# Performance work log

Measured on AMD Instinct MI355X. Metric: run time of the kernel, lower is better.

The kernel has to match this reference:

```python
import jax, jax.numpy as jnp
import numpy as np

EPS = 1e-5
K = 16
DILATION = 1

def _bn(x, g, b, axes):
    # BatchNorm in training mode: batch statistics over all axes except channel (last)
    m = jnp.mean(x, axis=axes, keepdims=True)
    v = jnp.var(x, axis=axes, keepdims=True)
    return (x - m) * jax.lax.rsqrt(v + EPS) * g + b

def _knn_idx(p, q, k):
    # p: [B,N,3], q: [B,M,3] -> indices [B,M,k] of nearest points in p for each q
    d = (jnp.sum(q * q, -1)[:, :, None]
         - 2.0 * jnp.einsum('bmc,bnc->bmn', q, p)
         + jnp.sum(p * p, -1)[:, None, :])  # [B,M,N]
    _, idx = jax.lax.top_k(-d, k)
    return jax.lax.stop_gradient(idx)

def setup_inputs() -> dict:
    key = jax.random.key(0)
    ks = jax.random.split(key, 16)
    B, N, M, Cin, Cout = 8, 8192, 2048, 64, 128
    mid, K2 = Cout // 4, K * K
    s = 0.02
    d = {
        'p': jax.random.normal(ks[0], (B, N, 3), jnp.float32),
        'q': jax.random.normal(ks[1], (B, M, 3), jnp.float32),
        'x': jax.random.normal(ks[2], (B, Cin, N), jnp.float32),
        # mlp: two 1x1 convs (3->mid->mid) each with BN
        'W1': jax.random.normal(ks[3], (mid, 3), jnp.float32) * s,
        'b1': jnp.zeros((mid,), jnp.float32),
        'g1': jnp.ones((mid,), jnp.float32), 'be1': jnp.zeros((mid,), jnp.float32),
        'W2': jax.random.normal(ks[4], (mid, mid), jnp.float32) * s,
        'b2': jnp.zeros((mid,), jnp.float32),
        'g2': jnp.ones((mid,), jnp.float32), 'be2': jnp.zeros((mid,), jnp.float32),
        # stn: conv [1,K] (3->K^2), then two 1x1 convs (K^2->K^2)
        'Ws1': jax.random.normal(ks[5], (K2, 3, K), jnp.float32) * s,
        'bs1': jnp.zeros((K2,), jnp.float32),
        'gs1': jnp.ones((K2,), jnp.float32), 'bes1': jnp.zeros((K2,), jnp.float32),
        'Ws2': jax.random.normal(ks[6], (K2, K2), jnp.float32) * s,
        'bs2': jnp.zeros((K2,), jnp.float32),
        'gs2': jnp.ones((K2,), jnp.float32), 'bes2': jnp.zeros((K2,), jnp.float32),
        'Ws3': jax.random.normal(ks[7], (K2, K2), jnp.float32) * s,
        'bs3': jnp.zeros((K2,), jnp.float32),
        # final conv [1,K]: (Cin+mid -> Cout) with BN
        'Wc': jax.random.normal(ks[8], (Cout, Cin + mid, K), jnp.float32) * s,
        'bc': jnp.zeros((Cout,), jnp.float32),
        'gc': jnp.ones((Cout,), jnp.float32), 'bec': jnp.zeros((Cout,), jnp.float32),
    }
    return d

def reference(p, q, x, W1, b1, g1, be1, W2, b2, g2, be2,
              Ws1, bs1, gs1, bes1, Ws2, bs2, gs2, bes2, Ws3, bs3,
              Wc, bc, gc, bec):
    B, M = q.shape[0], q.shape[1]
    idx = _knn_idx(p, q, K * DILATION)[..., ::DILATION]  # [B,M,K]
    # gather neighbor coords and center: p_hat [B,M,K,3]
    p_n = jax.vmap(lambda a, i: a[i])(p, idx)
    p_hat = p_n - q[:, :, None, :]
    # mlp (pointwise convs, channel-last)
    h = jax.nn.relu(_bn(jnp.einsum('bmkc,oc->bmko', p_hat, W1) + b1, g1, be1, (0, 1, 2)))
    h = jax.nn.relu(_bn(jnp.einsum('bmkc,oc->bmko', h, W2) + b2, g2, be2, (0, 1, 2)))
    # gather features: x [B,Cin,N] -> [B,M,K,Cin]
    xt = jnp.transpose(x, (0, 2, 1))
    x_n = jax.vmap(lambda a, i: a[i])(xt, idx)
    x_hat = jnp.concatenate([h, x_n], axis=-1)  # [B,M,K,mid+Cin]
    # stn -> transform T [B,M,K,K]
    t = jax.nn.relu(_bn(jnp.einsum('bmkc,ock->bmo', p_hat, Ws1) + bs1, gs1, bes1, (0, 1)))
    t = jax.nn.relu(_bn(jnp.einsum('bmi,oi->bmo', t, Ws2) + bs2, gs2, bes2, (0, 1)))
    t = jnp.einsum('bmi,oi->bmo', t, Ws3) + bs3  # [B,M,K*K]
    T = t.reshape(B, M, K, K)
    x2 = jnp.einsum('bmij,bmjc->bmic', T, x_hat)  # [B,M,K,mid+Cin]
    out = jax.nn.relu(_bn(jnp.einsum('bmkc,ock->bmo', x2, Wc) + bc, gc, bec, (0, 1)))  # [B,M,Cout]
    return (q, jnp.transpose(out, (0, 2, 1)))  # q, x:[B,Cout,M]
```

## Files before the change

kernel.cpp:

```cpp
#include <hip/hip_runtime.h>
#include <hip/hip_bf16.h>


#define EPS 1e-5f

constexpr int Bb   = 8;
constexpr int Np   = 8192;
constexpr int Mq   = 2048;
constexpr int COUT = 128;
constexpr int BM   = Bb * Mq;
constexpr int BMK  = BM * 16;
constexpr int GC   = 16;
constexpr int NC   = GC * GC * GC;
constexpr int CAP  = 320;
constexpr int TS   = 20;

typedef __attribute__((ext_vector_type(8))) short short8;
typedef __attribute__((ext_vector_type(4))) float f32x4;

__device__ __forceinline__ unsigned short f2bf(float x) {
  unsigned u = __float_as_uint(x);
  u += 0x7fffu + ((u >> 16) & 1u);
  return (unsigned short)(u >> 16);
}
__device__ __forceinline__ float bf2f_lo(unsigned v) { return __uint_as_float(v << 16); }
__device__ __forceinline__ float bf2f_hi(unsigned v) { return __uint_as_float(v & 0xffff0000u); }
__device__ __forceinline__ float bfround(float x) {
  return __uint_as_float(((unsigned)f2bf(x)) << 16);
}

__device__ __forceinline__ int cell_of(float c) {
  int v = (int)floorf(c * 2.0f + 8.0f);
  return v < 0 ? 0 : (v > 15 ? 15 : v);
}

__device__ __forceinline__ unsigned enc_dist(float d) {
  unsigned uu = __float_as_uint(d);
  return uu ^ (((unsigned)(((int)uu) >> 31)) | 0x80000000u);
}

__device__ __forceinline__ void bsort64(unsigned long long& v, int lane) {
#pragma unroll
  for (int k = 2; k <= 64; k <<= 1) {
#pragma unroll
    for (int jj = k >> 1; jj > 0; jj >>= 1) {
      unsigned long long o = __shfl_xor(v, jj);
      bool keepMin = (((lane & k) == 0) == ((lane & jj) == 0));
      unsigned long long mn = v < o ? v : o;
      unsigned long long mx = v < o ? o : v;
      v = keepMin ? mn : mx;
    }
  }
}
__device__ __forceinline__ void bmerge64(unsigned long long& v, int lane) {
#pragma unroll
  for (int jj = 32; jj > 0; jj >>= 1) {
    unsigned long long o = __shfl_xor(v, jj);
    bool keepMin = ((lane & jj) == 0);
    unsigned long long mn = v < o ? v : o;
    unsigned long long mx = v < o ? o : v;
    v = keepMin ? mn : mx;
  }
}
__device__ __forceinline__ unsigned long long sort_smallest64(const unsigned long long* buf,
                                                              int C, int lane) {
  unsigned long long run = (lane < C) ? buf[lane] : ~0ULL;
  bsort64(run, lane);
  for (int b2 = 64; b2 < C; b2 += 64) {
    unsigned long long v = (b2 + lane < C) ? buf[b2 + lane] : ~0ULL;
    bsort64(v, lane);
    unsigned long long vr = __shfl_xor(v, 63);
    unsigned long long m = run < vr ? run : vr;
    bmerge64(m, lane);
    run = m;
  }
  return run;
}


__device__ __forceinline__ void bn1_compute(int o, const float* __restrict__ st,
                                            const float* __restrict__ W1,
                                            const float* __restrict__ b1,
                                            const float* __restrict__ g1,
                                            const float* __restrict__ be1,
                                            float* sc_out, float* shf_out) {
  float n = (float)BMK;
  float w0 = W1[3 * o], w1 = W1[3 * o + 1], w2 = W1[3 * o + 2], b = b1[o];
  float s0 = st[0], s1 = st[1], s2 = st[2];
  float m00 = st[3], m11 = st[4], m22 = st[5], m01 = st[6], m02 = st[7], m12 = st[8];
  float ws = (w0 * s0 + w1 * s1 + w2 * s2) / n;
  float mean = b + ws;
  float quad = w0 * w0 * m00 + w1 * w1 * m11 + w2 * w2 * m22 +
               2.f * (w0 * w1 * m01 + w0 * w2 * m02 + w1 * w2 * m12);
  float ex2 = quad / n + 2.f * b * ws + b * b;
  float var = ex2 - mean * mean;
  float sc = g1[o] * rsqrtf(var + EPS);
  *sc_out = sc;
  *shf_out = be1[o] - mean * sc + b * sc;
}

__global__ __launch_bounds__(256) void prep_kernel(const float* __restrict__ p,
                                                   const float* __restrict__ x,
                                                   const float* __restrict__ Wc,
                                                   const float* __restrict__ Ws1,
                                                   float4* __restrict__ pp4,
                                                   float* __restrict__ xt,
                                                   unsigned short* __restrict__ wcrp,
                                                   unsigned short* __restrict__ ws1r,
                                                   int* __restrict__ hist) {
  __shared__ float tile[64][65];
  int blk = blockIdx.x;
  int tid = threadIdx.x;
  if (blk < 256) {
    int i = blk * 256 + tid;
    float px = p[3 * i], py = p[3 * i + 1], pz = p[3 * i + 2];
    float pp = __fadd_rn(__fadd_rn(__fmul_rn(px, px), __fmul_rn(py, py)), __fmul_rn(pz, pz));
    pp4[i] = make_float4(px, py, pz, pp);
    int b = i >> 13;
    int cid = (cell_of(px) << 8) | (cell_of(py) << 4) | cell_of(pz);
    atomicAdd(&hist[b * NC + cid], 1);
  } else if (blk < 1280) {
    int bx = blk - 256;
    int b = bx >> 7;
    int n0 = (bx & 127) << 6;
    int nl = tid & 63;
    int r0 = tid >> 6;
    const float* xb = x + (size_t)b * 64 * Np;
    for (int c = r0; c < 64; c += 4) tile[c][nl] = xb[(size_t)c * Np + n0 + nl];
    __syncthreads();
    float* xtb = xt + (size_t)b * Np * 64;
    for (int n = r0; n < 64; n += 4) xtb[(size_t)(n0 + n) * 64 + nl] = tile[nl][n];
  } else if (blk < 2048) {
    int g = (blk - 1280) * 256 + tid;
    if (g < 128 * 1536) {
      int o = g / 1536, r = g % 1536;
      int c = r % 96, j = r / 96;
      wcrp[g] = f2bf(Wc[(size_t)o * 1536 + c * 16 + j]);
    }
  } else {
    int g = (blk - 2048) * 256 + tid;
    int o = g >> 6, i = g & 63;
    float val = 0.f;
    if (i < 48) {
      int k = i / 3, c = i - 3 * k;
      val = Ws1[(size_t)o * 48 + c * 16 + k];
    }
    unsigned short h = f2bf(val);
    float hf = __uint_as_float(((unsigned)h) << 16);
    unsigned short l = f2bf(val - hf);
    ws1r[g] = h;
    ws1r[16384 + g] = l;
  }
}

__global__ __launch_bounds__(256) void prefix_kernel(const int* __restrict__ hist,
                                                     int* __restrict__ cellstart,
                                                     int* __restrict__ cursor) {
  __shared__ int ls[256];
  int b = blockIdx.x, t = threadIdx.x;
  const int* h = hist + b * NC;
  int loc[16], s = 0;
#pragma unroll
  for (int k = 0; k < 16; ++k) { loc[k] = h[t * 16 + k]; s += loc[k]; }
  ls[t] = s;
  __syncthreads();
  for (int off = 1; off < 256; off <<= 1) {
    int v = (t >= off) ? ls[t - off] : 0;
    __syncthreads();
    ls[t] += v;
    __syncthreads();
  }
  int run = ls[t] - s;
  int* cs = cellstart + b * (NC + 1);
  int* cu = cursor + b * NC;
#pragma unroll
  for (int k = 0; k < 16; ++k) {
    cs[t * 16 + k] = run;
    cu[t * 16 + k] = run;
    run += loc[k];
  }
  if (t == 255) cs[NC] = run;
}

__global__ __launch_bounds__(256) void scatter_kernel(const float4* __restrict__ pp4,
                                                      int* __restrict__ cursor,
                                                      float4* __restrict__ sp4,
                                                      int* __restrict__ sidx) {
  int i = blockIdx.x * 256 + threadIdx.x;
  int b = i >> 13;
  float4 pv = pp4[i];
  int cid = (cell_of(pv.x) << 8) | (cell_of(pv.y) << 4) | cell_of(pv.z);
  int pos = atomicAdd(&cursor[b * NC + cid], 1);
  sp4[(size_t)b * Np + pos] = pv;
  sidx[(size_t)b * Np + pos] = i & 8191;
}

__global__ __launch_bounds__(256) void knn_kernel(const float4* __restrict__ pp4,
                                                  const float4* __restrict__ sp4,
                                                  const int* __restrict__ sidx,
                                                  const int* __restrict__ cellstart,
                                                  const float* __restrict__ q,
                                                  int* __restrict__ idx_out) {
  __shared__ unsigned long long cand[4][CAP];
  int tid = threadIdx.x;
  int wslot = tid >> 6;
  int qi = blockIdx.x * 4 + wslot;
  int lane = tid & 63;
  int b = qi >> 11;
  const float4* pb = pp4 + (size_t)b * Np;
  const float4* sp = sp4 + (size_t)b * Np;
  const int* sx = sidx + (size_t)b * Np;
  const int* cs = cellstart + b * (NC + 1);
  const float* qp = q + (size_t)qi * 3;
  float qx = qp[0], qy = qp[1], qz = qp[2];
  float qqv = __fadd_rn(__fadd_rn(__fmul_rn(qx, qx), __fmul_rn(qy, qy)), __fmul_rn(qz, qz));
  float tau_f = INFINITY;

  {
    int cx = cell_of(qx), cy = cell_of(qy), cz = cell_of(qz);
    int alo = 0, blo = 0, nbw = 1, ncols = 1, zlo = 0, zhi = 0;
    int myS = 0, myE = 0;
    for (int r = 0;; ++r) {
      alo = cx - r; if (alo < 0) alo = 0;
      int ahi = cx + r; if (ahi > 15) ahi = 15;
      blo = cy - r; if (blo < 0) blo = 0;
      int bhi = cy + r; if (bhi > 15) bhi = 15;
      zlo = cz - r; if (zlo < 0) zlo = 0;
      zhi = cz + r; if (zhi > 15) zhi = 15;
      nbw = bhi - blo + 1;
      ncols = (ahi - alo + 1) * nbw;
      int total = 0;
      for (int l0 = 0; l0 < ncols; l0 += 64) {
        int l = l0 + lane;
        int sL = 0, eL = 0;
        if (l < ncols) {
          int da = l / nbw, db = l - da * nbw;
          int cbase = ((alo + da) << 8) | ((blo + db) << 4);
          sL = cs[cbase + zlo];
          eL = cs[cbase + zhi + 1];
        }
        if (l0 == 0) { myS = sL; myE = eL; }
        total += eL - sL;
      }
#pragma unroll
      for (int o = 32; o > 0; o >>= 1) total += __shfl_xor(total, o);
      if (total >= 16 || r >= 15) break;
    }
    unsigned u0 = 0xFFFFFFFFu, u1 = 0xFFFFFFFFu;
    int wcnt = 0;
    int ccen = (cx - alo) * nbw + (cy - blo);
    for (int c2 = 0; c2 < ncols && wcnt < 128; ++c2) {
      int cc = (c2 == 0) ? ccen : (c2 <= ccen ? c2 - 1 : c2);
      int s0, e;
      if (cc < 64) {
        s0 = __shfl(myS, cc);
        e = __shfl(myE, cc);
      } else {
        int da = cc / nbw, db = cc - da * nbw;
        int cbase = ((alo + da) << 8) | ((blo + db) << 4);
        s0 = cs[cbase + zlo];
        e = cs[cbase + zhi + 1];
      }
      for (int off = s0; off < e && wcnt < 128; off += 64) {
        int rem = e - off; if (rem > 64) rem = 64;
        int rot = wcnt & 63;
        int rel = (lane - rot) & 63;
        int g = wcnt + rel;
        if (rel < rem && g < 128) {
          float4 pv = sp[off + rel];
          float ee = __fmaf_rn(qz, pv.z, __fmaf_rn(qy, pv.y, __fmul_rn(qx, pv.x)));
          float d = __fadd_rn(__fsub_rn(qqv, __fmul_rn(2.0f, ee)), pv.w);
          unsigned uu = enc_dist(d);
          if (g < 64) u0 = uu; else u1 = uu;
        }
        wcnt += rem;
      }
    }
    unsigned lo = 0u, hi = 0xFF800000u;
    for (int it = 0; it < 20; ++it) {
      unsigned mid = lo + ((hi - lo) >> 1);
      int c = (int)__popcll(__ballot(u0 <= mid)) + (int)__popcll(__ballot(u1 <= mid));
      if (c >= 16) hi = mid; else lo = mid + 1;
    }
    tau_f = (hi >= 0x80000000u) ? __uint_as_float(hi ^ 0x80000000u)
                                : __uint_as_float(~hi);
  }

  int cnt = 0;
  unsigned long long lanebelow = (1ULL << lane) - 1ULL;
  {
    float R = sqrtf(fmaxf(tau_f, 0.f) + 3e-5f) * 1.0005f;
    int ax0 = cell_of(qx - R), ax1 = cell_of(qx + R);
    int ay0 = cell_of(qy - R), ay1 = cell_of(qy + R);
    int az0 = cell_of(qz - R), az1 = cell_of(qz + R);
    int nby = ay1 - ay0 + 1;
    int ncols = (ax1 - ax0 + 1) * nby;
    int myS = 0, myE = 0;
    if (lane < ncols) {
      int da = lane / nby, db = lane - da * nby;
      int cbase = ((ax0 + da) << 8) | ((ay0 + db) << 4);
      myS = cs[cbase + az0];
      myE = cs[cbase + az1 + 1];
    }
    for (int cc = 0; cc < ncols; ++cc) {
      int s0, e;
      if (cc < 64) {
        s0 = __shfl(myS, cc);
        e = __shfl(myE, cc);
      } else {
        int da = cc / nby, db = cc - da * nby;
        int cbase = ((ax0 + da) << 8) | ((ay0 + db) << 4);
        s0 = cs[cbase + az0];
        e = cs[cbase + az1 + 1];
      }
      for (int off = s0; off < e; off += 64) {
        int pos = off + lane;
        bool valid = pos < e;
        float4 pv = sp[valid ? pos : s0];
        float ee = __fmaf_rn(qz, pv.z, __fmaf_rn(qy, pv.y, __fmul_rn(qx, pv.x)));
        float d = __fadd_rn(__fsub_rn(qqv, __fmul_rn(2.0f, ee)), pv.w);
        if (!valid) d = __uint_as_float(0x7FC00000u);
        unsigned long long mask = __ballot(d <= tau_f);
        if (mask) {
          if (d <= tau_f) {
            int oi = sx[pos];
            unsigned uu = enc_dist(d);
            int wp = cnt + (int)__popcll(mask & lanebelow);
            if (wp < CAP)
              cand[wslot][wp] = (((unsigned long long)uu) << 32) | (unsigned)oi;
          }
          cnt += (int)__popcll(mask);
        }
      }
    }
  }
  __syncthreads();

  if (cnt <= CAP) {
    unsigned long long run = sort_smallest64(&cand[wslot][0], cnt, lane);
    if (lane < 16)
      idx_out[(size_t)qi * 16 + lane] = (int)(run & 0xffffffffULL);
  } else {
    unsigned long long kk = ~0ULL;
    float tl = tau_f;
    for (int base = 0; base < Np; base += 64) {
      float4 pv = pb[base + lane];
      float ee = __fmaf_rn(qz, pv.z, __fmaf_rn(qy, pv.y, __fmul_rn(qx, pv.x)));
      float dv = __fadd_rn(__fsub_rn(qqv, __fmul_rn(2.0f, ee)), pv.w);
      unsigned long long mask = __ballot(dv <= tl);
      if (mask) {
        unsigned uu = enc_dist(dv);
        unsigned long long cd = (((unsigned long long)uu) << 32) | (unsigned)(base + lane);
        do {
          int src = __ffsll((unsigned long long)mask) - 1;
          mask &= mask - 1;
          unsigned long long ck = __shfl(cd, src);
          unsigned long long up = __shfl_up(kk, 1);
          if (lane == 0) up = 0ULL;
          if (lane < 16 && ck < kk) kk = (up > ck) ? up : ck;
        } while (mask);
        unsigned long long tt = __shfl(kk, 15);
        unsigned tm = (unsigned)(tt >> 32);
        unsigned inv2 = tm ^ ((tm & 0x80000000u) ? 0x80000000u : 0xFFFFFFFFu);
        float tc = (tm == 0xFFFFFFFFu) ? INFINITY : __uint_as_float(inv2);
        if (tc < tl) tl = tc;
      }
    }
    if (lane < 16)
      idx_out[(size_t)qi * 16 + lane] = (int)(kk & 0xffffffffULL);
  }
}

__global__ __launch_bounds__(256) void phat_stats_kernel(const float4* __restrict__ pp4,
                                                         const float* __restrict__ q,
                                                         const int* __restrict__ idx,
                                                         float* __restrict__ phat,
                                                         float* __restrict__ stats) {
  float a[9];
#pragma unroll
  for (int k = 0; k < 9; ++k) a[k] = 0.f;
  int tid = threadIdx.x;
  for (int it = 0; it < 4; ++it) {
    int bmk = blockIdx.x * 256 + tid + it * 65536;
    int bm = bmk >> 4;
    int b = bm >> 11;
    int j = idx[bmk];
    float4 pv = pp4[(size_t)b * Np + j];
    const float* qp = q + (size_t)bm * 3;
    float h0 = pv.x - qp[0], h1 = pv.y - qp[1], h2 = pv.z - qp[2];
    phat[(size_t)bmk * 3 + 0] = h0;
    phat[(size_t)bmk * 3 + 1] = h1;
    phat[(size_t)bmk * 3 + 2] = h2;
    a[0] += h0; a[1] += h1; a[2] += h2;
    a[3] += h0 * h0; a[4] += h1 * h1; a[5] += h2 * h2;
    a[6] += h0 * h1; a[7] += h0 * h2; a[8] += h1 * h2;
  }
#pragma unroll
  for (int off = 32; off > 0; off >>= 1)
#pragma unroll
    for (int k = 0; k < 9; ++k) a[k] += __shfl_down(a[k], off);
  __shared__ float ls[9];
  if (tid < 9) ls[tid] = 0.f;
  __syncthreads();
  if ((tid & 63) == 0)
    for (int k = 0; k < 9; ++k) atomicAdd(&ls[k], a[k]);
  __syncthreads();
  if (tid < 9) atomicAdd(&stats[tid], ls[tid]);
}

__global__ __launch_bounds__(256) void stats2_kernel(const float* __restrict__ phat,
                                                     const float* __restrict__ stats,
                                                     const float* __restrict__ W1,
                                                     const float* __restrict__ b1,
                                                     const float* __restrict__ g1,
                                                     const float* __restrict__ be1,
                                                     const float* __restrict__ W2,
                                                     const float* __restrict__ b2,
                                                     float* __restrict__ stats2) {
  __shared__ float hsh[256 * 36];
  __shared__ float w2s[32 * 33];
  __shared__ float w1s[96], sc1[32], sh1[32], b2s[32], ls[64];
  int tid = threadIdx.x;
  if (tid < 32) {
    bn1_compute(tid, stats, W1, b1, g1, be1, &sc1[tid], &sh1[tid]);
    b2s[tid] = b2[tid];
  }
  if (tid < 96) w1s[tid] = W1[tid];
  if (tid < 64) ls[tid] = 0.f;
  for (int e = tid; e < 1024; e += 256) w2s[(e >> 5) * 33 + (e & 31)] = W2[e];
  __syncthreads();
  {
    int bmk = blockIdx.x * 256 + tid;
    float h0 = phat[(size_t)bmk * 3], hy = phat[(size_t)bmk * 3 + 1], hz = phat[(size_t)bmk * 3 + 2];
#pragma unroll
    for (int o4 = 0; o4 < 8; ++o4) {
      float4 r;
      float* rp = (float*)&r;
#pragma unroll
      for (int u = 0; u < 4; ++u) {
        int o = o4 * 4 + u;
        float t = w1s[3 * o] * h0 + w1s[3 * o + 1] * hy + w1s[3 * o + 2] * hz;
        rp[u] = fmaxf(0.f, t * sc1[o] + sh1[o]);
      }
      *(float4*)&hsh[tid * 36 + o4 * 4] = r;
    }
  }
  __syncthreads();
  int oc = tid & 31, grp = tid >> 5;
  float wrow[32];
#pragma unroll
  for (int c = 0; c < 32; ++c) wrow[c] = w2s[oc * 33 + c];
  float bias = b2s[oc];
  float ss = 0.f, qq = 0.f;
  for (int r = 0; r < 32; ++r) {
    int row = grp * 32 + r;
    float a = bias;
    const float4* hr = (const float4*)&hsh[row * 36];
#pragma unroll
    for (int c4 = 0; c4 < 8; ++c4) {
      float4 hv = hr[c4];
      a += hv.x * wrow[c4 * 4 + 0];
      a += hv.y * wrow[c4 * 4 + 1];
      a += hv.z * wrow[c4 * 4 + 2];
      a += hv.w * wrow[c4 * 4 + 3];
    }
    ss += a;
    qq += a * a;
  }
  atomicAdd(&ls[oc], ss);
  atomicAdd(&ls[32 + oc], qq);
  __syncthreads();
  if (tid < 64) atomicAdd(&stats2[tid], ls[tid]);
}

__global__ __launch_bounds__(256) void stn1_kernel(const float* __restrict__ phat,
                                                   const unsigned short* __restrict__ ws1r,
                                                   const float* __restrict__ bs1,
                                                   float* __restrict__ pt1,
                                                   float* __restrict__ spt1) {
  __shared__ unsigned short Ah[64 * 72], Al[64 * 72], Bh[128 * 72], Bl[128 * 72];
  __shared__ float ls[256];
  int tid = threadIdx.x;
  ls[tid] = 0.f;
  int mb = blockIdx.x >> 1, nb = blockIdx.x & 1;
  int bm0 = mb * 64, o0 = nb * 128;
  {
    int zr = tid >> 2, zc = 48 + (tid & 3) * 4;
    *(unsigned long long*)&Ah[zr * 72 + zc] = 0ULL;
    *(unsigned long long*)&Al[zr * 72 + zc] = 0ULL;
  }
  {
    int ar = tid >> 2, aseg = tid & 3;
    const float* Ap = phat + (size_t)(bm0 + ar) * 48 + aseg * 12;
    float4 v0 = *(const float4*)(Ap);
    float4 v1 = *(const float4*)(Ap + 4);
    float4 v2 = *(const float4*)(Ap + 8);
    float av[12] = {v0.x, v0.y, v0.z, v0.w, v1.x, v1.y, v1.z, v1.w, v2.x, v2.y, v2.z, v2.w};
    unsigned long long ph[3] = {0ULL, 0ULL, 0ULL}, pl[3] = {0ULL, 0ULL, 0ULL};
#pragma unroll
    for (int t = 0; t < 12; ++t) {
      unsigned short h = f2bf(av[t]);
      float hf = __uint_as_float(((unsigned)h) << 16);
      unsigned short l = f2bf(av[t] - hf);
      ph[t >> 2] |= ((unsigned long long)h) << ((t & 3) * 16);
      pl[t >> 2] |= ((unsigned long long)l) << ((t & 3) * 16);
    }
    int base = ar * 72 + aseg * 12;
#pragma unroll
    for (int t4 = 0; t4 < 3; ++t4) {
      *(unsigned long long*)&Ah[base + t4 * 4] = ph[t4];
      *(unsigned long long*)&Al[base + t4 * 4] = pl[t4];
    }
  }
#pragma unroll
  for (int pass = 0; pass < 4; ++pass) {
    int g = pass * 2048 + tid * 8;
    int br = g >> 6, i2 = g & 63;
    short8 vh = *(const short8*)&ws1r[(size_t)(o0 + br) * 64 + i2];
    short8 vl = *(const short8*)&ws1r[16384 + (size_t)(o0 + br) * 64 + i2];
    *(short8*)&Bh[br * 72 + i2] = vh;
    *(short8*)&Bl[br * 72 + i2] = vl;
  }
  __syncthreads();
  int wid = tid >> 6, lane = tid & 63;
  int wm = wid >> 1, wn = wid & 1;
  int mh = lane & 15, quad = lane >> 4;
  f32x4 acc[2][4];
#pragma unroll
  for (int a = 0; a < 2; ++a)
#pragma unroll
    for (int bq = 0; bq < 4; ++bq) acc[a][bq] = (f32x4){0.f, 0.f, 0.f, 0.f};
#pragma unroll
  for (int kc = 0; kc < 2; ++kc) {
    int ko = kc * 32 + quad * 8;
#pragma unroll
    for (int mt = 0; mt < 2; ++mt) {
      short8 ah = *(const short8*)&Ah[(wm * 32 + mt * 16 + mh) * 72 + ko];
      short8 al = *(const short8*)&Al[(wm * 32 + mt * 16 + mh) * 72 + ko];
#pragma unroll
      for (int nt = 0; nt < 4; ++nt) {
        short8 bh = *(const short8*)&Bh[(wn * 64 + nt * 16 + mh) * 72 + ko];
        short8 bl = *(const short8*)&Bl[(wn * 64 + nt * 16 + mh) * 72 + ko];
        acc[mt][nt] = __builtin_amdgcn_mfma_f32_16x16x32_bf16(ah, bh, acc[mt][nt], 0, 0, 0);
        acc[mt][nt] = __builtin_amdgcn_mfma_f32_16x16x32_bf16(ah, bl, acc[mt][nt], 0, 0, 0);
        acc[mt][nt] = __builtin_amdgcn_mfma_f32_16x16x32_bf16(al, bh, acc[mt][nt], 0, 0, 0);
      }
    }
  }
#pragma unroll
  for (int mt = 0; mt < 2; ++mt)
#pragma unroll
    for (int nt = 0; nt < 4; ++nt) {
      int colL = wn * 64 + nt * 16 + mh;
      int col = o0 + colL;
      float bvv = bs1[col];
      float ps = 0.f, pq = 0.f;
#pragma unroll
      for (int r = 0; r < 4; ++r) {
        float val = acc[mt][nt][r] + bvv;
        pt1[(size_t)(bm0 + wm * 32 + mt * 16 + quad * 4 + r) * 256 + col] = val;
        ps += val;
        pq += val * val;
      }
      atomicAdd(&ls[colL], ps);
      atomicAdd(&ls[128 + colL], pq);
    }
  __syncthreads();
  if (tid < 128) {
    atomicAdd(&spt1[o0 + tid], ls[tid]);
    atomicAdd(&spt1[256 + o0 + tid], ls[128 + tid]);
  }
}

__global__ __launch_bounds__(256) void stn_mm_kernel(const float* __restrict__ in,
                                                     const float* __restrict__ sums,
                                                     const float* __restrict__ gg,
                                                     const float* __restrict__ be,
                                                     const float* __restrict__ W,
                                                     const float* __restrict__ bias,
                                                     float* __restrict__ out,
                                                     float* __restrict__ outstats,
                                                     int do_stats) {
  __shared__ unsigned short As[64 * 40], Bs[128 * 40];
  __shared__ float scA[256], shA[256], ls[256];
  int tid = threadIdx.x;
  ls[tid] = 0.f;
  {
    float n = (float)BM;
    float mean = sums[tid] / n;
    float var = sums[256 + tid] / n - mean * mean;
    float s = gg[tid] * rsqrtf(var + EPS);
    scA[tid] = s;
    shA[tid] = be[tid] - mean * s;
  }
  int mb = blockIdx.x >> 1, nb = blockIdx.x & 1;
  int bm0 = mb * 64, o0 = nb * 128;
  int wid = tid >> 6, lane = tid & 63;
  int wm = wid >> 1, wn = wid & 1;
  int mh = lane & 15, quad = lane >> 4;
  f32x4 acc[2][4];
#pragma unroll
  for (int a = 0; a < 2; ++a)
#pragma unroll
    for (int bq = 0; bq < 4; ++bq) acc[a][bq] = (f32x4){0.f, 0.f, 0.f, 0.f};
  int ar = tid >> 2, aseg = tid & 3;
  const float* Ag = in + (size_t)(bm0 + ar) * 256 + aseg * 8;
  int aoff = ar * 40 + aseg * 8;
  int ci = aseg * 8;
  for (int i0 = 0; i0 < 256; i0 += 32) {
    __syncthreads();
    float4 v0 = *(const float4*)(Ag + i0);
    float4 v1 = *(const float4*)(Ag + i0 + 4);
    float av[8] = {v0.x, v0.y, v0.z, v0.w, v1.x, v1.y, v1.z, v1.w};
    short8 ap;
#pragma unroll
    for (int k = 0; k < 8; ++k)
      ap[k] = (short)f2bf(fmaxf(0.f, av[k] * scA[i0 + ci + k] + shA[i0 + ci + k]));
    *(short8*)&As[aoff] = ap;
#pragma unroll
    for (int jb = 0; jb < 2; ++jb) {
      int br = jb * 64 + ar;
      const float* Bg = W + (size_t)(o0 + br) * 256 + aseg * 8;
      float4 u0 = *(const float4*)(Bg + i0);
      float4 u1 = *(const float4*)(Bg + i0 + 4);
      float bv[8] = {u0.x, u0.y, u0.z, u0.w, u1.x, u1.y, u1.z, u1.w};
      short8 bp;
#pragma unroll
      for (int k = 0; k < 8; ++k) bp[k] = (short)f2bf(bv[k]);
      *(short8*)&Bs[br * 40 + aseg * 8] = bp;
    }
    __syncthreads();
#pragma unroll
    for (int mt = 0; mt < 2; ++mt) {
      short8 af = *(const short8*)&As[(wm * 32 + mt * 16 + mh) * 40 + quad * 8];
#pragma unroll
      for (int nt = 0; nt < 4; ++nt) {
        short8 bf = *(const short8*)&Bs[(wn * 64 + nt * 16 + mh) * 40 + quad * 8];
        acc[mt][nt] = __builtin_amdgcn_mfma_f32_16x16x32_bf16(af, bf, acc[mt][nt], 0, 0, 0);
      }
    }
  }
#pragma unroll
  for (int mt = 0; mt < 2; ++mt)
#pragma unroll
    for (int nt = 0; nt < 4; ++nt) {
      int colL = wn * 64 + nt * 16 + mh;
      int col = o0 + colL;
      float bvv = bias[col];
      float ps = 0.f, pq = 0.f;
#pragma unroll
      for (int r = 0; r < 4; ++r) {
        float val = acc[mt][nt][r] + bvv;
        out[(size_t)(bm0 + wm * 32 + mt * 16 + quad * 4 + r) * 256 + col] = val;
        ps += val;
        pq += val * val;
      }
      if (do_stats) {
        atomicAdd(&ls[colL], ps);
        atomicAdd(&ls[128 + colL], pq);
      }
    }
  if (do_stats) {
    __syncthreads();
    if (tid < 128) {
      atomicAdd(&outstats[o0 + tid], ls[tid]);
      atomicAdd(&outstats[256 + o0 + tid], ls[128 + tid]);
    }
  }
}

__global__ __launch_bounds__(256) void xhat_x2_kernel(const float* __restrict__ phat,
                                                      const float* __restrict__ stats,
                                                      const float* __restrict__ stats2,
                                                      const float* __restrict__ W1,
                                                      const float* __restrict__ b1,
                                                      const float* __restrict__ g1,
                                                      const float* __restrict__ be1,
                                                      const float* __restrict__ W2,
                                                      const float* __restrict__ b2,
                                                      const float* __restrict__ g2,
                                                      const float* __restrict__ be2,
                                                      const float* __restrict__ xt,
                                                      const int* __restrict__ idx,
                                                      const float* __restrict__ Tbuf,
                                                      unsigned short* __restrict__ x2) {
  __shared__ unsigned xh[256 * 17];
  __shared__ float Tst[256 * TS];
  __shared__ float sc1[32], sh1[32], sc2[32], sh2[32];
  int tid = threadIdx.x;
  if (tid < 32) {
    bn1_compute(tid, stats, W1, b1, g1, be1, &sc1[tid], &sh1[tid]);
    float n = (float)BMK;
    float mean = stats2[tid] / n;
    float var = stats2[32 + tid] / n - mean * mean;
    float s = g2[tid] * rsqrtf(var + EPS);
    sc2[tid] = s;
    sh2[tid] = be2[tid] - mean * s + b2[tid] * s;
  }
  __syncthreads();
  int bm0 = blockIdx.x * 16;
  int b = bm0 >> 11;
  int bml = tid >> 4, j = tid & 15;
  int bmk = (bm0 + bml) * 16 + j;
  int jxr[16];
  {
    const int* idxrow = idx + (size_t)(bm0 + bml) * 16;
#pragma unroll
    for (int jj = 0; jj < 16; ++jj) jxr[jj] = idxrow[jj];
  }
  {
    float h0 = phat[(size_t)bmk * 3], hy = phat[(size_t)bmk * 3 + 1], hz = phat[(size_t)bmk * 3 + 2];
    float h1v[32];
#pragma unroll
    for (int o = 0; o < 32; ++o) {
      float t = W1[3 * o] * h0 + W1[3 * o + 1] * hy + W1[3 * o + 2] * hz;
      h1v[o] = fmaxf(0.f, t * sc1[o] + sh1[o]);
    }
#pragma unroll
    for (int o4 = 0; o4 < 8; ++o4) {
      float r[4];
#pragma unroll
      for (int u = 0; u < 4; ++u) {
        int o = o4 * 4 + u;
        float a = 0.f;
#pragma unroll
        for (int c = 0; c < 32; ++c) a += h1v[c] * W2[o * 32 + c];
        r[u] = fmaxf(0.f, a * sc2[o] + sh2[o]);
      }
      xh[tid * 17 + o4 * 2] = (unsigned)f2bf(r[0]) | (((unsigned)f2bf(r[1])) << 16);
      xh[tid * 17 + o4 * 2 + 1] = (unsigned)f2bf(r[2]) | (((unsigned)f2bf(r[3])) << 16);
    }
    const float4* tg = (const float4*)(Tbuf + (size_t)(bm0 + bml) * 256 + j * 16);
    float4* td = (float4*)&Tst[tid * TS];
    td[0] = tg[0]; td[1] = tg[1]; td[2] = tg[2]; td[3] = tg[3];
  }
  __syncthreads();
  int cl = j;
  {
    float vlo[16], vhi[16];
#pragma unroll
    for (int jj = 0; jj < 16; ++jj) {
      unsigned uv = xh[(bml * 16 + jj) * 17 + cl];
      vlo[jj] = bf2f_lo(uv);
      vhi[jj] = bf2f_hi(uv);
    }
    for (int jo = 0; jo < 16; ++jo) {
      const float4* tr4 = (const float4*)&Tst[(bml * 16 + jo) * TS];
      float4 ta = tr4[0], tb = tr4[1], tc = tr4[2], tdd = tr4[3];
      float trow[16] = {ta.x, ta.y, ta.z, ta.w, tb.x, tb.y, tb.z, tb.w,
                        tc.x, tc.y, tc.z, tc.w, tdd.x, tdd.y, tdd.z, tdd.w};
      float a0 = 0.f, a1 = 0.f;
#pragma unroll
      for (int jj = 0; jj < 16; ++jj) {
        a0 += trow[jj] * vlo[jj];
        a1 += trow[jj] * vhi[jj];
      }
      unsigned* dst = (unsigned*)(x2 + (size_t)((bm0 + bml) * 16 + jo) * 96);
      dst[cl] = (unsigned)f2bf(a0) | (((unsigned)f2bf(a1)) << 16);
    }
  }
  {
    float v0[16], v1[16], v2[16], v3[16];
#pragma unroll
    for (int jj = 0; jj < 16; ++jj) {
      int jx = jxr[jj];
      float4 xv = *(const float4*)(xt + ((size_t)b * Np + jx) * 64 + cl * 4);
      v0[jj] = bfround(xv.x);
      v1[jj] = bfround(xv.y);
      v2[jj] = bfround(xv.z);
      v3[jj] = bfround(xv.w);
    }
    for (int jo = 0; jo < 16; ++jo) {
      const float4* tr4 = (const float4*)&Tst[(bml * 16 + jo) * TS];
      float4 ta = tr4[0], tb = tr4[1], tc = tr4[2], tdd = tr4[3];
      float trow[16] = {ta.x, ta.y, ta.z, ta.w, tb.x, tb.y, tb.z, tb.w,
                        tc.x, tc.y, tc.z, tc.w, tdd.x, tdd.y, tdd.z, tdd.w};
      float a0 = 0.f, a1 = 0.f, a2 = 0.f, a3 = 0.f;
#pragma unroll
      for (int jj = 0; jj < 16; ++jj) {
        float t = trow[jj];
        a0 += t * v0[jj];
        a1 += t * v1[jj];
        a2 += t * v2[jj];
        a3 += t * v3[jj];
      }
      unsigned* dst = (unsigned*)(x2 + (size_t)((bm0 + bml) * 16 + jo) * 96);
      dst[16 + cl * 2] = (unsigned)f2bf(a0) | (((unsigned)f2bf(a1)) << 16);
      dst[17 + cl * 2] = (unsigned)f2bf(a2) | (((unsigned)f2bf(a3)) << 16);
    }
  }
}

__global__ __launch_bounds__(256) void preout_kernel(const unsigned short* __restrict__ x2,
                                                     const unsigned short* __restrict__ Wcrp,
                                                     const float* __restrict__ bc,
                                                     float* __restrict__ pout,
                                                     float* __restrict__ spout) {
  __shared__ unsigned short As[64 * 40], Bs[128 * 40];
  __shared__ float ls[256];
  int tid = threadIdx.x;
  ls[tid] = 0.f;
  int bm0 = blockIdx.x * 64;
  int wid = tid >> 6, lane = tid & 63;
  int wm = wid >> 1, wn = wid & 1;
  int mh = lane & 15, quad = lane >> 4;
  f32x4 acc[2][4];
#pragma unroll
  for (int a = 0; a < 2; ++a)
#pragma unroll
    for (int bq = 0; bq < 4; ++bq) acc[a][bq] = (f32x4){0.f, 0.f, 0.f, 0.f};
  int ar = tid >> 2, aseg = tid & 3;
  const unsigned short* Ag = x2 + (size_t)(bm0 + ar) * 1536 + aseg * 8;
  const unsigned short* Bg0 = Wcrp + (size_t)ar * 1536 + aseg * 8;
  const unsigned short* Bg1 = Wcrp + (size_t)(64 + ar) * 1536 + aseg * 8;
  int aoff = ar * 40 + aseg * 8;
  short8 a_pre = *(const short8*)Ag;
  short8 b_pre0 = *(const short8*)Bg0;
  short8 b_pre1 = *(const short8*)Bg1;
  for (int i0 = 0; i0 < 1536; i0 += 32) {
    __syncthreads();
    *(short8*)&As[aoff] = a_pre;
    *(short8*)&Bs[aoff] = b_pre0;
    *(short8*)&Bs[64 * 40 + aoff] = b_pre1;
    __syncthreads();
    if (i0 + 32 < 1536) {
      a_pre = *(const short8*)(Ag + i0 + 32);
      b_pre0 = *(const short8*)(Bg0 + i0 + 32);
      b_pre1 = *(const short8*)(Bg1 + i0 + 32);
    }
#pragma unroll
    for (int mt = 0; mt < 2; ++mt) {
      short8 af = *(const short8*)&As[(wm * 32 + mt * 16 + mh) * 40 + quad * 8];
#pragma unroll
      for (int nt = 0; nt < 4; ++nt) {
        short8 bf = *(const short8*)&Bs[(wn * 64 + nt * 16 + mh) * 40 + quad * 8];
        acc[mt][nt] = __builtin_amdgcn_mfma_f32_16x16x32_bf16(af, bf, acc[mt][nt], 0, 0, 0);
      }
    }
  }
#pragma unroll
  for (int mt = 0; mt < 2; ++mt)
#pragma unroll
    for (int nt = 0; nt < 4; ++nt) {
      int col = wn * 64 + nt * 16 + mh;
      float bvv = bc[col];
      float ps = 0.f, pq = 0.f;
#pragma unroll
      for (int r = 0; r < 4; ++r) {
        float val = acc[mt][nt][r] + bvv;
        pout[(size_t)(bm0 + wm * 32 + mt * 16 + quad * 4 + r) * 128 + col] = val;
        ps += val;
        pq += val * val;
      }
      atomicAdd(&ls[col], ps);
      atomicAdd(&ls[128 + col], pq);
    }
  __syncthreads();
  atomicAdd(&spout[tid], ls[tid]);
}

__global__ __launch_bounds__(256) void final_kernel(const float* __restrict__ q,
                                                    const float* __restrict__ pout,
                                                    const float* __restrict__ scs,
                                                    const float* __restrict__ gc,
                                                    const float* __restrict__ bec,
                                                    float* __restrict__ dout) {
  __shared__ float ldsT[128 * 65];
  int blk = blockIdx.x;
  int tid = threadIdx.x;
  if (blk < 192) {
    int g = blk * 256 + tid;
    dout[g] = q[g];
    return;
  }
  int blk2 = blk - 192;
  int b = blk2 >> 5;
  int m0 = (blk2 & 31) * 64;
  int row = tid >> 2, seg = tid & 3;
  const float4* src = (const float4*)(pout + ((size_t)(b * Mq) + m0 + row) * 128 + seg * 32);
#pragma unroll
  for (int k4 = 0; k4 < 8; ++k4) {
    float4 v = src[k4];
    int o = seg * 32 + k4 * 4;
    ldsT[(o + 0) * 65 + row] = v.x;
    ldsT[(o + 1) * 65 + row] = v.y;
    ldsT[(o + 2) * 65 + row] = v.z;
    ldsT[(o + 3) * 65 + row] = v.w;
  }
  __syncthreads();
  int lane = tid & 63, wv = tid >> 6;
  float n = (float)BM;
  float* base = dout + (size_t)BM * 3 + (size_t)b * COUT * Mq + m0;
#pragma unroll
  for (int rep = 0; rep < 32; ++rep) {
    int o = wv * 32 + rep;
    float mean = scs[o] / n;
    float var = scs[128 + o] / n - mean * mean;
    float s = gc[o] * rsqrtf(var + EPS);
    float shv = bec[o] - mean * s;
    float v = ldsT[o * 65 + lane];
    base[(size_t)o * Mq + lane] = fmaxf(0.f, v * s + shv);
  }
}

extern "C" void kernel_launch(void* const* d_in, const int* in_sizes, int n_in, void* d_out,
                              int out_size, void* d_ws, size_t ws_size, hipStream_t stream) {
  const float* p = (const float*)d_in[0];
  const float* q = (const float*)d_in[1];
  const float* x = (const float*)d_in[2];
  const float* W1 = (const float*)d_in[3];
  const float* b1 = (const float*)d_in[4];
  const float* g1 = (const float*)d_in[5];
  const float* be1 = (const float*)d_in[6];
  const float* W2 = (const float*)d_in[7];
  const float* b2 = (const float*)d_in[8];
  const float* g2 = (const float*)d_in[9];
  const float* be2 = (const float*)d_in[10];
  const float* Ws1 = (const float*)d_in[11];
  const float* bs1 = (const float*)d_in[12];
  const float* gs1 = (const float*)d_in[13];
  const float* bes1 = (const float*)d_in[14];
  const float* Ws2 = (const float*)d_in[15];
  const float* bs2 = (const float*)d_in[16];
  const float* gs2 = (const float*)d_in[17];
  const float* bes2 = (const float*)d_in[18];
  const float* Ws3 = (const float*)d_in[19];
  const float* bs3 = (const float*)d_in[20];
  const float* Wc = (const float*)d_in[21];
  const float* bc = (const float*)d_in[22];
  const float* gc = (const float*)d_in[23];
  const float* bec = (const float*)d_in[24];
  float* dout = (float*)d_out;

  char* ws = (char*)d_ws;
  float* stats = (float*)ws;
  size_t off = 8192;
  float4* pp4 = (float4*)(ws + off);  off += (size_t)Bb * Np * 16;
  int* idxb = (int*)(ws + off);       off += (size_t)BMK * 4;
  float* xt = (float*)(ws + off);     off += (size_t)Bb * Np * 64 * 4;
  float* phat = (float*)(ws + off);   off += (size_t)BMK * 3 * 4;
  float* pt1 = (float*)(ws + off);    off += (size_t)BM * 256 * 4;
  float* pt2 = (float*)(ws + off);    off += (size_t)BM * 256 * 4;
  float* Tb = (float*)(ws + off);     off += (size_t)BM * 256 * 4;
  float* pout = (float*)(ws + off);   off += (size_t)BM * 128 * 4;
  unsigned short* wcrp = (unsigned short*)(ws + off); off += (size_t)1536 * 128 * 2;
  unsigned short* x2 = (unsigned short*)(ws + off);   off += (size_t)BM * 1536 * 2;
  int* hist = (int*)(ws + off);       off += (size_t)Bb * NC * 4;
  int* cursor = (int*)(ws + off);     off += (size_t)Bb * NC * 4;
  int* cellstart = (int*)(ws + off);  off += (size_t)Bb * (NC + 1) * 4;
  float4* sp4 = (float4*)(ws + off);  off += (size_t)Bb * Np * 16;
  int* sidx = (int*)(ws + off);       off += (size_t)Bb * Np * 4;
  unsigned short* ws1r = (unsigned short*)(ws + off); off += (size_t)2 * 256 * 64 * 2;

  hipMemsetAsync(stats, 0, 8192, stream);
  hipMemsetAsync(hist, 0, (size_t)Bb * NC * 4, stream);
  hipLaunchKernelGGL(prep_kernel, dim3(2112), dim3(256), 0, stream, p, x, Wc, Ws1, pp4, xt, wcrp, ws1r, hist);
  hipLaunchKernelGGL(prefix_kernel, dim3(8), dim3(256), 0, stream, hist, cellstart, cursor);
  hipLaunchKernelGGL(scatter_kernel, dim3(256), dim3(256), 0, stream, pp4, cursor, sp4, sidx);
  hipLaunchKernelGGL(knn_kernel, dim3(4096), dim3(256), 0, stream, pp4, sp4, sidx, cellstart, q, idxb);
  hipLaunchKernelGGL(phat_stats_kernel, dim3(256), dim3(256), 0, stream, pp4, q, idxb, phat, stats);
  hipLaunchKernelGGL(stn1_kernel, dim3(512), dim3(256), 0, stream, phat, ws1r, bs1, pt1, stats + 128);
  hipLaunchKernelGGL(stats2_kernel, dim3(1024), dim3(256), 0, stream, phat, stats, W1, b1, g1, be1, W2, b2, stats + 16);
  hipLaunchKernelGGL(stn_mm_kernel, dim3(512), dim3(256), 0, stream, pt1, stats + 128, gs1, bes1, Ws2, bs2, pt2, stats + 640, 1);
  hipLaunchKernelGGL(stn_mm_kernel, dim3(512), dim3(256), 0, stream, pt2, stats + 640, gs2, bes2, Ws3, bs3, Tb, (float*)nullptr, 0);
  hipLaunchKernelGGL(xhat_x2_kernel, dim3(1024), dim3(256), 0, stream, phat, stats, stats + 16,
                     W1, b1, g1, be1, W2, b2, g2, be2, xt, idxb, Tb, x2);
  hipLaunchKernelGGL(preout_kernel, dim3(256), dim3(256), 0, stream, x2, wcrp, bc, pout, stats + 1152);
  hipLaunchKernelGGL(final_kernel, dim3(448), dim3(256), 0, stream, q, pout, stats + 1152, gc, bec, dout);
}
```

Before: 355.7 us.

## Fuse phat computation into kNN, one query per block, move q copy to prep

The kNN kernel now runs one wave per block (64 threads, 16384 blocks) and computes the centred neighbour coordinates (phat) for its 16 results right away. This drops the separate gather pass in phat_stats_kernel, which now only reads phat to accumulate statistics. The copy of q into the output moves from final_kernel into extra prep_kernel blocks. Single-wave blocks remove the block-wide sync and let waves with slow queries retire independently, at the cost of more block launches and some redundant work per block.

```diff
diff --git a/kernel.cpp b/kernel.cpp
--- a/kernel.cpp
+++ b/kernel.cpp
@@ -103,11 +103,13 @@
                                                    const float* __restrict__ x,
                                                    const float* __restrict__ Wc,
                                                    const float* __restrict__ Ws1,
+                                                   const float* __restrict__ q,
                                                    float4* __restrict__ pp4,
                                                    float* __restrict__ xt,
                                                    unsigned short* __restrict__ wcrp,
                                                    unsigned short* __restrict__ ws1r,
-                                                   int* __restrict__ hist) {
+                                                   int* __restrict__ hist,
+                                                   float* __restrict__ dout) {
   __shared__ float tile[64][65];
   int blk = blockIdx.x;
   int tid = threadIdx.x;
@@ -137,7 +139,7 @@
       int c = r % 96, j = r / 96;
       wcrp[g] = f2bf(Wc[(size_t)o * 1536 + c * 16 + j]);
     }
-  } else {
+  } else if (blk < 2112) {
     int g = (blk - 2048) * 256 + tid;
     int o = g >> 6, i = g & 63;
     float val = 0.f;
@@ -150,6 +152,9 @@
     unsigned short l = f2bf(val - hf);
     ws1r[g] = h;
     ws1r[16384 + g] = l;
+  } else {
+    int g = (blk - 2112) * 256 + tid;
+    dout[g] = q[g];
   }
 }
 
@@ -195,17 +200,16 @@
   sidx[(size_t)b * Np + pos] = i & 8191;
 }
 
-__global__ __launch_bounds__(256) void knn_kernel(const float4* __restrict__ pp4,
-                                                  const float4* __restrict__ sp4,
-                                                  const int* __restrict__ sidx,
-                                                  const int* __restrict__ cellstart,
-                                                  const float* __restrict__ q,
-                                                  int* __restrict__ idx_out) {
-  __shared__ unsigned long long cand[4][CAP];
-  int tid = threadIdx.x;
-  int wslot = tid >> 6;
-  int qi = blockIdx.x * 4 + wslot;
-  int lane = tid & 63;
+__global__ __launch_bounds__(64) void knn_kernel(const float4* __restrict__ pp4,
+                                                 const float4* __restrict__ sp4,
+                                                 const int* __restrict__ sidx,
+                                                 const int* __restrict__ cellstart,
+                                                 const float* __restrict__ q,
+                                                 int* __restrict__ idx_out,
+                                                 float* __restrict__ phat) {
+  __shared__ unsigned long long cand[CAP];
+  int lane = threadIdx.x;
+  int qi = blockIdx.x;
   int b = qi >> 11;
   const float4* pb = pp4 + (size_t)b * Np;
   const float4* sp = sp4 + (size_t)b * Np;
@@ -327,19 +331,17 @@
             unsigned uu = enc_dist(d);
             int wp = cnt + (int)__popcll(mask & lanebelow);
             if (wp < CAP)
-              cand[wslot][wp] = (((unsigned long long)uu) << 32) | (unsigned)oi;
+              cand[wp] = (((unsigned long long)uu) << 32) | (unsigned)oi;
           }
           cnt += (int)__popcll(mask);
         }
       }
     }
   }
-  __syncthreads();
-
+
+  unsigned long long key16 = ~0ULL;
   if (cnt <= CAP) {
-    unsigned long long run = sort_smallest64(&cand[wslot][0], cnt, lane);
-    if (lane < 16)
-      idx_out[(size_t)qi * 16 + lane] = (int)(run & 0xffffffffULL);
+    key16 = sort_smallest64(&cand[0], cnt, lane);
   } else {
     unsigned long long kk = ~0ULL;
     float tl = tau_f;
@@ -366,15 +368,21 @@
         if (tc < tl) tl = tc;
       }
     }
-    if (lane < 16)
-      idx_out[(size_t)qi * 16 + lane] = (int)(kk & 0xffffffffULL);
-  }
-}
-
-__global__ __launch_bounds__(256) void phat_stats_kernel(const float4* __restrict__ pp4,
-                                                         const float* __restrict__ q,
-                                                         const int* __restrict__ idx,
-                                                         float* __restrict__ phat,
+    key16 = kk;
+  }
+  if (lane < 16) {
+    int oi = (int)(key16 & 0xffffffffULL);
+    idx_out[(size_t)qi * 16 + lane] = oi;
+    float4 pv = pb[oi];
+    float h0 = pv.x - qx, h1 = pv.y - qy, h2 = pv.z - qz;
+    size_t base3 = ((size_t)qi * 16 + lane) * 3;
+    phat[base3 + 0] = h0;
+    phat[base3 + 1] = h1;
+    phat[base3 + 2] = h2;
+  }
+}
+
+__global__ __launch_bounds__(256) void phat_stats_kernel(const float* __restrict__ phat,
                                                          float* __restrict__ stats) {
   float a[9];
 #pragma unroll
@@ -382,15 +390,9 @@
   int tid = threadIdx.x;
   for (int it = 0; it < 4; ++it) {
     int bmk = blockIdx.x * 256 + tid + it * 65536;
-    int bm = bmk >> 4;
-    int b = bm >> 11;
-    int j = idx[bmk];
-    float4 pv = pp4[(size_t)b * Np + j];
-    const float* qp = q + (size_t)bm * 3;
-    float h0 = pv.x - qp[0], h1 = pv.y - qp[1], h2 = pv.z - qp[2];
-    phat[(size_t)bmk * 3 + 0] = h0;
-    phat[(size_t)bmk * 3 + 1] = h1;
-    phat[(size_t)bmk * 3 + 2] = h2;
+    float h0 = phat[(size_t)bmk * 3 + 0];
+    float h1 = phat[(size_t)bmk * 3 + 1];
+    float h2 = phat[(size_t)bmk * 3 + 2];
     a[0] += h0; a[1] += h1; a[2] += h2;
     a[3] += h0 * h0; a[4] += h1 * h1; a[5] += h2 * h2;
     a[6] += h0 * h1; a[7] += h0 * h2; a[8] += h1 * h2;
@@ -859,21 +861,14 @@
   atomicAdd(&spout[tid], ls[tid]);
 }
 
-__global__ __launch_bounds__(256) void final_kernel(const float* __restrict__ q,
-                                                    const float* __restrict__ pout,
+__global__ __launch_bounds__(256) void final_kernel(const float* __restrict__ pout,
                                                     const float* __restrict__ scs,
                                                     const float* __restrict__ gc,
                                                     const float* __restrict__ bec,
                                                     float* __restrict__ dout) {
   __shared__ float ldsT[128 * 65];
-  int blk = blockIdx.x;
+  int blk2 = blockIdx.x;
   int tid = threadIdx.x;
-  if (blk < 192) {
-    int g = blk * 256 + tid;
-    dout[g] = q[g];
-    return;
-  }
-  int blk2 = blk - 192;
   int b = blk2 >> 5;
   int m0 = (blk2 & 31) * 64;
   int row = tid >> 2, seg = tid & 3;
@@ -954,11 +949,11 @@
 
   hipMemsetAsync(stats, 0, 8192, stream);
   hipMemsetAsync(hist, 0, (size_t)Bb * NC * 4, stream);
-  hipLaunchKernelGGL(prep_kernel, dim3(2112), dim3(256), 0, stream, p, x, Wc, Ws1, pp4, xt, wcrp, ws1r, hist);
+  hipLaunchKernelGGL(prep_kernel, dim3(2304), dim3(256), 0, stream, p, x, Wc, Ws1, q, pp4, xt, wcrp, ws1r, hist, dout);
   hipLaunchKernelGGL(prefix_kernel, dim3(8), dim3(256), 0, stream, hist, cellstart, cursor);
   hipLaunchKernelGGL(scatter_kernel, dim3(256), dim3(256), 0, stream, pp4, cursor, sp4, sidx);
-  hipLaunchKernelGGL(knn_kernel, dim3(4096), dim3(256), 0, stream, pp4, sp4, sidx, cellstart, q, idxb);
-  hipLaunchKernelGGL(phat_stats_kernel, dim3(256), dim3(256), 0, stream, pp4, q, idxb, phat, stats);
+  hipLaunchKernelGGL(knn_kernel, dim3(16384), dim3(64), 0, stream, pp4, sp4, sidx, cellstart, q, idxb, phat);
+  hipLaunchKernelGGL(phat_stats_kernel, dim3(256), dim3(256), 0, stream, phat, stats);
   hipLaunchKernelGGL(stn1_kernel, dim3(512), dim3(256), 0, stream, phat, ws1r, bs1, pt1, stats + 128);
   hipLaunchKernelGGL(stats2_kernel, dim3(1024), dim3(256), 0, stream, phat, stats, W1, b1, g1, be1, W2, b2, stats + 16);
   hipLaunchKernelGGL(stn_mm_kernel, dim3(512), dim3(256), 0, stream, pt1, stats + 128, gs1, bes1, Ws2, bs2, pt2, stats + 640, 1);
@@ -966,5 +961,5 @@
   hipLaunchKernelGGL(xhat_x2_kernel, dim3(1024), dim3(256), 0, stream, phat, stats, stats + 16,
                      W1, b1, g1, be1, W2, b2, g2, be2, xt, idxb, Tb, x2);
   hipLaunchKernelGGL(preout_kernel, dim3(256), dim3(256), 0, stream, x2, wcrp, bc, pout, stats + 1152);
-  hipLaunchKernelGGL(final_kernel, dim3(448), dim3(256), 0, stream, q, pout, stats + 1152, gc, bec, dout);
-}
+  hipLaunchKernelGGL(final_kernel, dim3(256), dim3(256), 0, stream, pout, stats + 1152, gc, bec, dout);
+}
```

Result: no change. 359.1 us (+1.0%).
